# Kernel tuning notes

Measured on AMD Instinct MI355X. Metric: run time of the kernel, lower is better.

## Reference

```python
import jax, jax.numpy as jnp
import numpy as np

N_NODES = 50000


def gcn_conv(x, W, b, row, col, n):
    """PyG GCNConv with default add_self_loops=True, normalize=True.
    out[i] = sum_{e: col[e]=i} d^-1/2[row[e]] d^-1/2[i] * (x@W)[row[e]]
             + d^-1[i]*(x@W)[i] + b,  where d = in-degree + 1 (self-loop).
    """
    x_lin = x @ W                                   # [n, out_ch]
    ones = jnp.ones(row.shape[0], dtype=x.dtype)
    deg = jax.ops.segment_sum(ones, col, num_segments=n) + 1.0  # self-loop
    dinv = jax.lax.rsqrt(deg)                       # deg >= 1, safe
    norm = dinv[row] * dinv[col]                    # [E]
    msg = norm[:, None] * x_lin[row]                # [E, out_ch]
    agg = jax.ops.segment_sum(msg, col, num_segments=n)
    self_term = (dinv * dinv)[:, None] * x_lin      # self-loop contribution
    return agg + self_term + b


def setup_inputs() -> dict:
    key = jax.random.key(0)
    ks = jax.random.split(key, 10)
    in_ch, hid, out_ch = 128, 256, 64
    E = 800000
    x = jax.random.normal(ks[0], (N_NODES, in_ch), dtype=jnp.float32)
    edge_attr = jax.random.normal(ks[1], (E, 8), dtype=jnp.float32)  # unused by forward
    edge_index = jax.random.randint(ks[2], (2, E), 0, N_NODES, dtype=jnp.int64)
    def glorot(k, fan_in, fan_out):
        s = float(np.sqrt(6.0 / (fan_in + fan_out)))
        return jax.random.uniform(k, (fan_in, fan_out), jnp.float32, -s, s)
    return {
        "x": x,
        "edge_attr": edge_attr,
        "edge_index": edge_index,
        "W1": glorot(ks[3], in_ch, hid), "b1": jnp.zeros((hid,), jnp.float32),
        "W2": glorot(ks[4], hid, hid),  "b2": jnp.zeros((hid,), jnp.float32),
        "W3": glorot(ks[5], hid, out_ch), "b3": jnp.zeros((out_ch,), jnp.float32),
    }


def reference(x, edge_attr, edge_index, W1, b1, W2, b2, W3, b3):
    n = x.shape[0]
    row, col = edge_index[0], edge_index[1]
    h = jax.nn.sigmoid(gcn_conv(x, W1, b1, row, col, n))
    h = jax.nn.sigmoid(gcn_conv(h, W2, b2, row, col, n))
    # dropout(p=0.1) in eval mode is identity
    return gcn_conv(h, W3, b3, row, col, n)
```

## Files before the change

### kernel.cpp

```cpp
#include <hip/hip_runtime.h>
#include <hip/hip_bf16.h>

typedef __bf16 bf16x8_t __attribute__((ext_vector_type(8)));
typedef float f32x4_t __attribute__((ext_vector_type(4)));
typedef float f32x2_t __attribute__((ext_vector_type(2)));

__device__ __forceinline__ float bits2f(unsigned int u) {
    union { unsigned int u; float f; } c; c.u = u; return c.f;
}
__device__ __forceinline__ unsigned short f2bf_bits(float f) {
    __hip_bfloat16 h = __float2bfloat16(f);
    return __builtin_bit_cast(unsigned short, h);
}
__device__ __forceinline__ f32x2_t unpack_bf2(unsigned int u) {
    return (f32x2_t){bits2f(u << 16), bits2f(u & 0xffff0000u)};
}
__device__ __forceinline__ int get_xcd() {
    unsigned v;
    asm volatile("s_getreg_b32 %0, hwreg(HW_REG_XCC_ID)" : "=s"(v));
    return (int)(v & 7);
}

__global__ void sentinel_fill(float* __restrict__ out, int n) {
    int i = blockIdx.x * blockDim.x + threadIdx.x;
    if (i < n) out[i] = 100.0f;
}

__global__ void init_combo(const unsigned int* __restrict__ ei, int* __restrict__ flags,
                           unsigned* __restrict__ cnt8, int Mln) {
    if (blockIdx.x == 0) {
        if (threadIdx.x < 64) {
            int lane = threadIdx.x;
            int cz = 0;
            #pragma unroll
            for (int j = 0; j < 4; ++j) {
                int idx = lane * 4 + j;
                cz += (ei[2 * idx + 1] == 0u);
            }
            #pragma unroll
            for (int off = 32; off; off >>= 1) cz += __shfl_down(cz, off);
            if (lane == 0) flags[0] = (cz > 200);
        }
    } else {
        int i = (blockIdx.x - 1) * 256 + threadIdx.x;
        if (i < Mln) cnt8[i] = 0u;
    }
}

__global__ void count_rank_xcd(const int* __restrict__ ei, unsigned* __restrict__ cnt8,
                               int* __restrict__ rank, int* __restrict__ c32,
                               int* __restrict__ r32, unsigned char* __restrict__ xcd8,
                               int E, int M, const int* __restrict__ flags) {
    int e = blockIdx.x * 256 + threadIdx.x;
    int xcd = get_xcd();
    if (e < E) {
        int r, c;
        if (flags[0]) { r = ei[2 * e]; c = ei[2 * E + 2 * e]; }
        else          { r = ei[e];     c = ei[E + e]; }
        c32[e] = c;
        r32[e] = r;
        xcd8[e] = (unsigned char)xcd;
        int rk = 0;
        if ((unsigned)c < (unsigned)M)
            rk = (int)__hip_atomic_fetch_add(&cnt8[(size_t)xcd * M + c], 1u,
                                             __ATOMIC_RELAXED, __HIP_MEMORY_SCOPE_WORKGROUP);
        rank[e] = rk;
    }
}

__global__ void scan_blocks_x(const unsigned* __restrict__ cnt8, unsigned* __restrict__ base8,
                              int* __restrict__ tot, int* __restrict__ excl,
                              int* __restrict__ bsum, int M) {
    int tid = threadIdx.x;
    int i = blockIdx.x * 256 + tid;
    int lane = tid & 63, wv = tid >> 6;
    __shared__ int ws[4];
    int v = 0;
    if (i < M) {
        unsigned run = 0;
        #pragma unroll
        for (int x = 0; x < 8; ++x) {
            unsigned cv = cnt8[(size_t)x * M + i];
            base8[(size_t)x * M + i] = run;
            run += cv;
        }
        v = (int)run;
        tot[i] = v;
    }
    int s = v;
    #pragma unroll
    for (int off = 1; off < 64; off <<= 1) {
        int t = __shfl_up(s, off);
        if (lane >= off) s += t;
    }
    if (lane == 63) ws[wv] = s;
    __syncthreads();
    if (tid == 0) { int a = 0; for (int q = 0; q < 4; ++q) { int t = ws[q]; ws[q] = a; a += t; } }
    __syncthreads();
    int ex = s - v + ws[wv];
    if (i < M) excl[i] = ex;
    if (tid == 255) bsum[blockIdx.x] = ex + v;
}

__global__ void scan_bsums(const int* __restrict__ bsum, int* __restrict__ boff,
                           int nb, int* __restrict__ colptr, int n) {
    int tid = threadIdx.x, lane = tid & 63, wv = tid >> 6;
    __shared__ int ws[4];
    __shared__ int carry;
    if (tid == 0) carry = 0;
    __syncthreads();
    for (int base = 0; base < nb; base += 256) {
        int i = base + tid;
        int v = (i < nb) ? bsum[i] : 0;
        int s = v;
        #pragma unroll
        for (int off = 1; off < 64; off <<= 1) {
            int t = __shfl_up(s, off);
            if (lane >= off) s += t;
        }
        if (lane == 63) ws[wv] = s;
        __syncthreads();
        if (tid == 0) { int a = carry; for (int q = 0; q < 4; ++q) { int t = ws[q]; ws[q] = a; a += t; } carry = a; }
        __syncthreads();
        int ex = s - v + ws[wv];
        if (i < nb) boff[i] = ex;
        __syncthreads();
    }
    if (tid == 0) colptr[n] = carry;
}

__global__ void scan_add_dinv(const int* __restrict__ excl, const int* __restrict__ boff,
                              const int* __restrict__ tot, int* __restrict__ colptr,
                              float* __restrict__ dinv, int n) {
    int i = blockIdx.x * 256 + threadIdx.x;
    if (i < n) {
        colptr[i] = excl[i] + boff[blockIdx.x];
        dinv[i] = rsqrtf((float)tot[i] + 1.0f);
    }
}

__global__ void fill_csr_part2(const int* __restrict__ c32, const int* __restrict__ r32,
                               const unsigned char* __restrict__ xcd8,
                               const unsigned* __restrict__ base8,
                               const int* __restrict__ colptr, const int* __restrict__ rank,
                               int* __restrict__ esrc, int E, int M, int psz) {
    int part = blockIdx.x & 7;
    int e = (blockIdx.x >> 3) * 256 + threadIdx.x;
    int lo = part * psz;
    int hi = lo + psz; if (hi > M) hi = M;
    if (e < E) {
        int c = c32[e];
        if (c >= lo && c < hi) {
            int r = r32[e];
            if ((unsigned)r < (unsigned)M) {
                int p = colptr[c] + (int)base8[(size_t)xcd8[e] * M + c] + rank[e];
                if ((unsigned)p < (unsigned)E) esrc[p] = r;
            }
        }
    }
}

__global__ void prep_fused(const float* __restrict__ x, const float* __restrict__ dinv,
                           unsigned char* __restrict__ xs8,
                           const float* __restrict__ W1, const float* __restrict__ W2,
                           const float* __restrict__ W3,
                           unsigned short* __restrict__ Wt1, unsigned short* __restrict__ Wt2,
                           unsigned short* __restrict__ Wt3,
                           int M, int nps) {
    if ((int)blockIdx.x < nps) {
        int i = blockIdx.x * 256 + threadIdx.x;
        if (i < M * 32) {
            int row = i >> 5;
            float dv = dinv[row];
            float4 v = *(const float4*)(x + (size_t)i * 4);
            unsigned u = __builtin_amdgcn_cvt_pk_fp8_f32(v.x * dv, v.y * dv, 0, false);
            u = __builtin_amdgcn_cvt_pk_fp8_f32(v.z * dv, v.w * dv, u, true);
            *(unsigned*)(xs8 + (size_t)i * 4) = u;
        }
    } else {
        int i = ((int)blockIdx.x - nps) * 256 + threadIdx.x;
        if (i < 32768) {
            int k = i >> 8, n = i & 255;
            Wt1[n * 128 + k] = f2bf_bits(W1[i]);
        } else if (i < 32768 + 65536) {
            int j = i - 32768;
            int k = j >> 8, n = j & 255;
            Wt2[n * 256 + k] = f2bf_bits(W2[j]);
        } else if (i < 114688) {
            int j = i - 98304;
            int k = j >> 6, n = j & 63;
            Wt3[n * 256 + k] = f2bf_bits(W3[j]);
        }
    }
}

template<int K, int BN, int NTOT, int EPI>
__global__ __launch_bounds__(256) void gemm_tile(
    const __bf16* __restrict__ A,
    const unsigned short* __restrict__ Bt,
    const float* __restrict__ dinv,
    const float* __restrict__ bias,
    void* __restrict__ Y,
    int M)
{
    constexpr int KS = (K > 128) ? 128 : K;
    constexpr int KP = KS + 8;
    constexpr int NT = BN / 2 / 16;
    __shared__ unsigned short Bs[BN * KP];

    const int tid  = threadIdx.x;
    const int lane = tid & 63;
    const int wave = tid >> 6;
    const int wm   = wave >> 1;
    const int wn   = wave & 1;
    const int quad = lane >> 4;
    const int l16  = lane & 15;
    const int n0   = blockIdx.y * BN;

    int mrow[4];
#pragma unroll
    for (int mt = 0; mt < 4; ++mt) {
        int r = blockIdx.x * 128 + wm * 64 + mt * 16 + l16;
        mrow[mt] = (r < M) ? r : (M - 1);
    }

    f32x4_t acc[4][NT];
#pragma unroll
    for (int mt = 0; mt < 4; ++mt)
#pragma unroll
        for (int t = 0; t < NT; ++t) acc[mt][t] = (f32x4_t){0.f, 0.f, 0.f, 0.f};

    const unsigned short* BsW = &Bs[(wn * (BN / 2)) * KP];

    for (int kh = 0; kh < K; kh += KS) {
        constexpr int CH = BN * KS / 8;
        for (int idx = tid; idx < CH; idx += 256) {
            int n  = idx / (KS / 8);
            int k8 = idx - n * (KS / 8);
            uint4 v = *(const uint4*)(Bt + (size_t)(n0 + n) * K + kh + k8 * 8);
            *(uint4*)&Bs[n * KP + k8 * 8] = v;
        }
        __syncthreads();

#pragma unroll
        for (int kc = 0; kc < KS; kc += 32) {
            bf16x8_t a[4], b[NT];
#pragma unroll
            for (int mt = 0; mt < 4; ++mt)
                a[mt] = *(const bf16x8_t*)(A + (size_t)mrow[mt] * K + kh + kc + quad * 8);
#pragma unroll
            for (int t = 0; t < NT; ++t)
                b[t] = *(const bf16x8_t*)&BsW[(t * 16 + l16) * KP + kc + quad * 8];
#pragma unroll
            for (int mt = 0; mt < 4; ++mt)
#pragma unroll
                for (int t = 0; t < NT; ++t)
                    acc[mt][t] = __builtin_amdgcn_mfma_f32_16x16x32_bf16(a[mt], b[t], acc[mt][t], 0, 0, 0);
        }
        if (kh + KS < K) __syncthreads();
    }

    float bv[NT];
    if constexpr (EPI == 1) {
#pragma unroll
        for (int t = 0; t < NT; ++t)
            bv[t] = bias[n0 + wn * (BN / 2) + t * 16 + l16];
    }

#pragma unroll
    for (int mt = 0; mt < 4; ++mt) {
        int rowbase = blockIdx.x * 128 + wm * 64 + mt * 16 + quad * 4;
#pragma unroll
        for (int r = 0; r < 4; ++r) {
            int rrow = rowbase + r;
            if (rrow < M) {
                if constexpr (EPI == 0) {
                    float dv = dinv[rrow];
#pragma unroll
                    for (int t = 0; t < NT; ++t) {
                        int ccol = n0 + wn * (BN / 2) + t * 16 + l16;
                        ((__hip_bfloat16*)Y)[(size_t)rrow * NTOT + ccol] =
                            __float2bfloat16(acc[mt][t][r] * dv);
                    }
                } else if constexpr (EPI == 1) {
#pragma unroll
                    for (int t = 0; t < NT; ++t) {
                        int ccol = n0 + wn * (BN / 2) + t * 16 + l16;
                        float o = acc[mt][t][r] + bv[t];
                        o = 1.f / (1.f + __expf(-o));
                        ((__hip_bfloat16*)Y)[(size_t)rrow * NTOT + ccol] = __float2bfloat16(o);
                    }
                } else {
                    float dv = dinv[rrow];
#pragma unroll
                    for (int t = 0; t < NT; ++t) {
                        int ccol = n0 + wn * (BN / 2) + t * 16 + l16;
                        float o = acc[mt][t][r] * dv;
                        int pk = __builtin_amdgcn_cvt_pk_fp8_f32(o, o, 0, false);
                        ((unsigned char*)Y)[(size_t)rrow * NTOT + ccol] = (unsigned char)(pk & 0xff);
                    }
                }
            }
        }
    }
}

__global__ __launch_bounds__(256) void aggregate_fp8_v4(
    const unsigned char* __restrict__ Y8,
    const int* __restrict__ colptr,
    const int* __restrict__ esrc,
    const float* __restrict__ dinv,
    const float* __restrict__ bias,
    unsigned short* __restrict__ H,
    int M, int Etot)
{
    const int lane = threadIdx.x & 63;
    const int wave = threadIdx.x >> 6;
    int node = blockIdx.x * 4 + wave;
    if (node >= M) return;

    int s = colptr[node];
    int e = colptr[node + 1];
    if (s < 0) s = 0;
    if (e > Etot) e = Etot;
    if (e < s) e = s;
    int n = e - s;

    const char* Yb = (const char*)Y8;
    const unsigned lb = (unsigned)(lane * 4);

    unsigned su = *(const unsigned*)(Yb + (((unsigned)node) << 8) + lb);

    f32x2_t a0 = {0.f, 0.f}, a1 = {0.f, 0.f};

    auto gather8 = [&](unsigned* u, int base) {
        #pragma unroll
        for (int k = 0; k < 8; ++k) {
            unsigned off = (((unsigned)esrc[s + base + k]) << 8) + lb;
            u[k] = *(const unsigned*)(Yb + off);
        }
    };
    auto acc8 = [&](const unsigned* u) {
        #pragma unroll
        for (int k = 0; k < 8; ++k) {
            a0 += __builtin_amdgcn_cvt_pk_f32_fp8(u[k], false);
            a1 += __builtin_amdgcn_cvt_pk_f32_fp8(u[k], true);
        }
    };

    unsigned ua[8], ub[8];
    int NB = n >> 3;
    if (NB > 0) {
        gather8(ua, 0);
        int i = 1;
        for (; i + 1 < NB; i += 2) {
            gather8(ub, i << 3);
            acc8(ua);
            gather8(ua, (i + 1) << 3);
            acc8(ub);
        }
        if (i < NB) {
            gather8(ub, i << 3);
            acc8(ua);
            acc8(ub);
        } else {
            acc8(ua);
        }
    }
    #pragma unroll 2
    for (int t = NB << 3; t < n; ++t) {
        unsigned off = (((unsigned)esrc[s + t]) << 8) + lb;
        unsigned u = *(const unsigned*)(Yb + off);
        a0 += __builtin_amdgcn_cvt_pk_f32_fp8(u, false);
        a1 += __builtin_amdgcn_cvt_pk_f32_fp8(u, true);
    }
    a0 += __builtin_amdgcn_cvt_pk_f32_fp8(su, false);
    a1 += __builtin_amdgcn_cvt_pk_f32_fp8(su, true);

    float dv = dinv[node];
    float4 bv = *(const float4*)(bias + lane * 4);
    float o0 = a0[0] * dv + bv.x;
    float o1 = a0[1] * dv + bv.y;
    float o2 = a1[0] * dv + bv.z;
    float o3 = a1[1] * dv + bv.w;
    o0 = 1.f / (1.f + __expf(-o0));
    o1 = 1.f / (1.f + __expf(-o1));
    o2 = 1.f / (1.f + __expf(-o2));
    o3 = 1.f / (1.f + __expf(-o3));
    uint2 st;
    st.x = (unsigned)f2bf_bits(o0) | ((unsigned)f2bf_bits(o1) << 16);
    st.y = (unsigned)f2bf_bits(o2) | ((unsigned)f2bf_bits(o3) << 16);
    *(uint2*)(H + (size_t)node * 256 + lane * 4) = st;
}

__global__ __launch_bounds__(256) void aggregate_xs8b(
    const unsigned char* __restrict__ X8,
    const int* __restrict__ colptr,
    const int* __restrict__ esrc,
    const float* __restrict__ dinv,
    unsigned short* __restrict__ xa,
    int M, int Etot)
{
    const int lane = threadIdx.x & 63;
    const int wave = threadIdx.x >> 6;
    const int l4 = lane & 15;
    const int g4 = lane >> 4;
    int node = blockIdx.x * 4 + wave;
    if (node >= M) return;

    int s = colptr[node];
    int e = colptr[node + 1];
    if (s < 0) s = 0;
    if (e > Etot) e = Etot;
    if (e < s) e = s;
    int n = e - s;

    const char* Yb = (const char*)X8;
    const unsigned lb = (unsigned)(l4 * 8);

    uint2 su = {0u, 0u};
    if (g4 == 0) su = *(const uint2*)(Yb + ((unsigned)node) * 128u + lb);

    f32x2_t a0 = {0.f, 0.f}, a1 = {0.f, 0.f}, a2 = {0.f, 0.f}, a3 = {0.f, 0.f};

    auto gat = [&](uint2* u, int base) {
        u[0] = *(const uint2*)(Yb + ((unsigned)esrc[s + base + g4]) * 128u + lb);
        u[1] = *(const uint2*)(Yb + ((unsigned)esrc[s + base + 4 + g4]) * 128u + lb);
    };
    auto acc = [&](const uint2* u) {
        #pragma unroll
        for (int k = 0; k < 2; ++k) {
            a0 += __builtin_amdgcn_cvt_pk_f32_fp8(u[k].x, false);
            a1 += __builtin_amdgcn_cvt_pk_f32_fp8(u[k].x, true);
            a2 += __builtin_amdgcn_cvt_pk_f32_fp8(u[k].y, false);
            a3 += __builtin_amdgcn_cvt_pk_f32_fp8(u[k].y, true);
        }
    };

    uint2 ua[2], ub[2];
    int NB = n >> 3;
    if (NB > 0) {
        gat(ua, 0);
        int i = 1;
        for (; i + 1 < NB; i += 2) {
            gat(ub, i << 3); acc(ua);
            gat(ua, (i + 1) << 3); acc(ub);
        }
        if (i < NB) { gat(ub, i << 3); acc(ua); acc(ub); }
        else acc(ua);
    }
    for (int t = NB << 3; t < n; t += 4) {
        if (t + g4 < n) {
            uint2 u = *(const uint2*)(Yb + ((unsigned)esrc[s + t + g4]) * 128u + lb);
            a0 += __builtin_amdgcn_cvt_pk_f32_fp8(u.x, false);
            a1 += __builtin_amdgcn_cvt_pk_f32_fp8(u.x, true);
            a2 += __builtin_amdgcn_cvt_pk_f32_fp8(u.y, false);
            a3 += __builtin_amdgcn_cvt_pk_f32_fp8(u.y, true);
        }
    }
    if (g4 == 0) {
        a0 += __builtin_amdgcn_cvt_pk_f32_fp8(su.x, false);
        a1 += __builtin_amdgcn_cvt_pk_f32_fp8(su.x, true);
        a2 += __builtin_amdgcn_cvt_pk_f32_fp8(su.y, false);
        a3 += __builtin_amdgcn_cvt_pk_f32_fp8(su.y, true);
    }

    #pragma unroll
    for (int off = 16; off < 64; off <<= 1) {
        a0[0] += __shfl_xor(a0[0], off); a0[1] += __shfl_xor(a0[1], off);
        a1[0] += __shfl_xor(a1[0], off); a1[1] += __shfl_xor(a1[1], off);
        a2[0] += __shfl_xor(a2[0], off); a2[1] += __shfl_xor(a2[1], off);
        a3[0] += __shfl_xor(a3[0], off); a3[1] += __shfl_xor(a3[1], off);
    }

    if (g4 == 0) {
        float dv = dinv[node];
        uint4 st;
        st.x = (unsigned)f2bf_bits(a0[0] * dv) | ((unsigned)f2bf_bits(a0[1] * dv) << 16);
        st.y = (unsigned)f2bf_bits(a1[0] * dv) | ((unsigned)f2bf_bits(a1[1] * dv) << 16);
        st.z = (unsigned)f2bf_bits(a2[0] * dv) | ((unsigned)f2bf_bits(a2[1] * dv) << 16);
        st.w = (unsigned)f2bf_bits(a3[0] * dv) | ((unsigned)f2bf_bits(a3[1] * dv) << 16);
        *(uint4*)(xa + (size_t)node * 128 + l4 * 8) = st;
    }
}

__global__ __launch_bounds__(256) void aggregate_bf16_64_v5(
    const unsigned short* __restrict__ Yin,
    const int* __restrict__ colptr,
    const int* __restrict__ esrc,
    const float* __restrict__ dinv,
    const float* __restrict__ bias,
    float* __restrict__ out,
    int M, int Etot)
{
    const int lane = threadIdx.x & 63;
    const int wave = threadIdx.x >> 6;
    const int l4 = lane & 15;
    const int g4 = lane >> 4;
    int node = blockIdx.x * 4 + wave;
    if (node >= M) return;

    int s = colptr[node];
    int e = colptr[node + 1];
    if (s < 0) s = 0;
    if (e > Etot) e = Etot;
    if (e < s) e = s;
    int n = e - s;

    const char* Yb = (const char*)Yin;
    const unsigned lb = (unsigned)(l4 * 8);

    uint2 su = {0u, 0u};
    if (g4 == 0) su = *(const uint2*)(Yb + ((unsigned)node) * 128u + lb);

    f32x2_t a0 = {0.f, 0.f}, a1 = {0.f, 0.f};

    auto gat = [&](uint2* u, int base) {
        u[0] = *(const uint2*)(Yb + ((unsigned)esrc[s + base + g4]) * 128u + lb);
        u[1] = *(const uint2*)(Yb + ((unsigned)esrc[s + base + 4 + g4]) * 128u + lb);
    };
    auto acc = [&](const uint2* u) {
        #pragma unroll
        for (int k = 0; k < 2; ++k) {
            a0 += unpack_bf2(u[k].x);
            a1 += unpack_bf2(u[k].y);
        }
    };

    uint2 ua[2], ub[2];
    int NB = n >> 3;
    if (NB > 0) {
        gat(ua, 0);
        int i = 1;
        for (; i + 1 < NB; i += 2) {
            gat(ub, i << 3); acc(ua);
            gat(ua, (i + 1) << 3); acc(ub);
        }
        if (i < NB) { gat(ub, i << 3); acc(ua); acc(ub); }
        else acc(ua);
    }
    for (int t = NB << 3; t < n; t += 4) {
        if (t + g4 < n) {
            uint2 u = *(const uint2*)(Yb + ((unsigned)esrc[s + t + g4]) * 128u + lb);
            a0 += unpack_bf2(u.x);
            a1 += unpack_bf2(u.y);
        }
    }
    if (g4 == 0) {
        a0 += unpack_bf2(su.x);
        a1 += unpack_bf2(su.y);
    }

    #pragma unroll
    for (int off = 16; off < 64; off <<= 1) {
        a0[0] += __shfl_xor(a0[0], off); a0[1] += __shfl_xor(a0[1], off);
        a1[0] += __shfl_xor(a1[0], off); a1[1] += __shfl_xor(a1[1], off);
    }

    if (g4 == 0) {
        float dv = dinv[node];
        float4 bv = *(const float4*)(bias + l4 * 4);
        float4 st;
        st.x = a0[0] * dv + bv.x;
        st.y = a0[1] * dv + bv.y;
        st.z = a1[0] * dv + bv.z;
        st.w = a1[1] * dv + bv.w;
        *(float4*)(out + (size_t)node * 64 + l4 * 4) = st;
    }
}


extern "C" void kernel_launch(void* const* d_in, const int* in_sizes, int n_in,
                              void* d_out, int out_size, void* d_ws, size_t ws_size,
                              hipStream_t stream)
{
    int iEI = 2, iW1 = 3, iB1 = 4, iW2 = 5, iB2 = 6, iW3 = 7, iB3 = 8;
    if (n_in == 8) { iEI = 1; iW1 = 2; iB1 = 3; iW2 = 4; iB2 = 5; iW3 = 6; iB3 = 7; }

    const float* x  = (const float*)d_in[0];
    const int* ei   = (const int*)d_in[iEI];
    const float* W1 = (const float*)d_in[iW1];
    const float* b1 = (const float*)d_in[iB1];
    const float* W2 = (const float*)d_in[iW2];
    const float* b2 = (const float*)d_in[iB2];
    const float* W3 = (const float*)d_in[iW3];
    const float* b3 = (const float*)d_in[iB3];

    const int M = in_sizes[0] / 128;
    const int E = in_sizes[iEI] / 2;
    const int NB = (M + 255) / 256;
    const int PSZ = (M + 7) / 8;

    auto rnd = [](size_t b) { return (b + 255) & ~(size_t)255; };
    size_t needed = rnd(64 * 4)
                  + rnd((size_t)M * 4)
                  + rnd((size_t)M * 32) * 2
                  + rnd((size_t)M * 4)
                  + rnd((size_t)(M + 1) * 4)
                  + rnd((size_t)M * 4)
                  + rnd((size_t)(NB + 1) * 4) * 2
                  + rnd((size_t)E * 4) * 4
                  + rnd((size_t)E)
                  + rnd((size_t)256 * 128 * 2)
                  + rnd((size_t)256 * 256 * 2)
                  + rnd((size_t)64 * 256 * 2)
                  + rnd((size_t)M * 256 * 2) * 2;
    if (ws_size < needed) {
        sentinel_fill<<<(out_size + 255) / 256, 256, 0, stream>>>((float*)d_out, out_size);
        return;
    }

    char* p = (char*)d_ws;
    auto alloc = [&](size_t bytes) {
        char* r = p;
        p += (bytes + 255) & ~(size_t)255;
        return r;
    };
    int* flags  = (int*)alloc(64 * 4);
    float* dinv = (float*)alloc((size_t)M * 4);
    unsigned* cnt8  = (unsigned*)alloc((size_t)M * 32);
    unsigned* base8 = (unsigned*)alloc((size_t)M * 32);
    int* tot    = (int*)alloc((size_t)M * 4);
    int* colptr = (int*)alloc((size_t)(M + 1) * 4);
    int* excl   = (int*)alloc((size_t)M * 4);
    int* bsum   = (int*)alloc((size_t)(NB + 1) * 4);
    int* boff   = (int*)alloc((size_t)(NB + 1) * 4);
    int* esrc   = (int*)alloc((size_t)E * 4);
    int* rank   = (int*)alloc((size_t)E * 4);
    int* c32    = (int*)alloc((size_t)E * 4);
    int* r32    = (int*)alloc((size_t)E * 4);
    unsigned char* xcd8 = (unsigned char*)alloc((size_t)E);
    unsigned short* Wt1 = (unsigned short*)alloc((size_t)256 * 128 * 2);
    unsigned short* Wt2 = (unsigned short*)alloc((size_t)256 * 256 * 2);
    unsigned short* Wt3 = (unsigned short*)alloc((size_t)64 * 256 * 2);
    __hip_bfloat16* ybuf = (__hip_bfloat16*)alloc((size_t)M * 256 * 2);
    __hip_bfloat16* hbuf = (__hip_bfloat16*)alloc((size_t)M * 256 * 2);

    unsigned char* xs8 = (unsigned char*)ybuf;
    unsigned short* xa = (unsigned short*)ybuf + (size_t)M * 128;
    unsigned char*  y8 = (unsigned char*)ybuf;

    int Mln = M * 8;
    init_combo<<<(Mln + 255) / 256 + 1, 256, 0, stream>>>(
        (const unsigned int*)ei, flags, cnt8, Mln);

    count_rank_xcd<<<(E + 255) / 256, 256, 0, stream>>>(
        ei, cnt8, rank, c32, r32, xcd8, E, M, flags);
    scan_blocks_x<<<NB, 256, 0, stream>>>(cnt8, base8, tot, excl, bsum, M);
    scan_bsums<<<1, 256, 0, stream>>>(bsum, boff, NB, colptr, M);
    scan_add_dinv<<<NB, 256, 0, stream>>>(excl, boff, tot, colptr, dinv, M);
    fill_csr_part2<<<((E + 255) / 256) * 8, 256, 0, stream>>>(
        c32, r32, xcd8, base8, colptr, rank, esrc, E, M, PSZ);

    int gmb = (M + 127) / 128;
    int ga  = (M + 3) / 4;
    int nps = (M * 32 + 255) / 256;

    prep_fused<<<nps + 448, 256, 0, stream>>>(
        x, dinv, xs8, W1, W2, W3, Wt1, Wt2, Wt3, M, nps);

    aggregate_xs8b<<<ga, 256, 0, stream>>>(
        xs8, colptr, esrc, dinv, xa, M, E);
    gemm_tile<128, 128, 256, 1><<<dim3(gmb, 2), 256, 0, stream>>>(
        (const __bf16*)xa, Wt1, dinv, b1, hbuf, M);
    gemm_tile<256, 128, 256, 2><<<dim3(gmb, 2), 256, 0, stream>>>(
        (const __bf16*)hbuf, Wt2, dinv, b2, y8, M);
    aggregate_fp8_v4<<<ga, 256, 0, stream>>>(
        y8, colptr, esrc, dinv, b2, (unsigned short*)hbuf, M, E);
    gemm_tile<256, 64, 64, 0><<<dim3(gmb, 1), 256, 0, stream>>>(
        (const __bf16*)hbuf, Wt3, dinv, b3, ybuf, M);
    aggregate_bf16_64_v5<<<ga, 256, 0, stream>>>(
        (const unsigned short*)ybuf, colptr, esrc, dinv, b3, (float*)d_out, M, E);
}
```

Measured before the change: 327.1 us.

## Fuse CSR fill into prep kernel and drop XCD-partitioned edge scatter

Merges the CSR edge-source fill into the x/weight preparation kernel, so one launch covers both jobs through disjoint block ranges. The fill previously launched 8x the blocks and had each partition handle only destination columns in its range, keeping scattered writes local to one XCD's cache. Now each edge is handled by exactly one block, which cuts redundant index loads and one launch. The cost is losing that per-XCD write locality for the esrc scatter.

```diff
diff --git a/kernel.cpp b/kernel.cpp
--- a/kernel.cpp
+++ b/kernel.cpp
@@ -139,36 +139,34 @@
     }
 }
 
-__global__ void fill_csr_part2(const int* __restrict__ c32, const int* __restrict__ r32,
-                               const unsigned char* __restrict__ xcd8,
-                               const unsigned* __restrict__ base8,
-                               const int* __restrict__ colptr, const int* __restrict__ rank,
-                               int* __restrict__ esrc, int E, int M, int psz) {
-    int part = blockIdx.x & 7;
-    int e = (blockIdx.x >> 3) * 256 + threadIdx.x;
-    int lo = part * psz;
-    int hi = lo + psz; if (hi > M) hi = M;
-    if (e < E) {
-        int c = c32[e];
-        if (c >= lo && c < hi) {
-            int r = r32[e];
-            if ((unsigned)r < (unsigned)M) {
-                int p = colptr[c] + (int)base8[(size_t)xcd8[e] * M + c] + rank[e];
-                if ((unsigned)p < (unsigned)E) esrc[p] = r;
+__global__ void fill_prep_fused(
+    const int* __restrict__ c32, const int* __restrict__ r32,
+    const unsigned char* __restrict__ xcd8, const unsigned* __restrict__ base8,
+    const int* __restrict__ colptr, const int* __restrict__ rank,
+    int* __restrict__ esrc, int E,
+    const float* __restrict__ x, const float* __restrict__ dinv,
+    unsigned char* __restrict__ xs8,
+    const float* __restrict__ W1, const float* __restrict__ W2,
+    const float* __restrict__ W3,
+    unsigned short* __restrict__ Wt1, unsigned short* __restrict__ Wt2,
+    unsigned short* __restrict__ Wt3,
+    int M, int nfe, int nps)
+{
+    int b = (int)blockIdx.x;
+    if (b < nfe) {
+        int e = b * 256 + threadIdx.x;
+        if (e < E) {
+            int c = c32[e];
+            if ((unsigned)c < (unsigned)M) {
+                int r = r32[e];
+                if ((unsigned)r < (unsigned)M) {
+                    int p = colptr[c] + (int)base8[(size_t)xcd8[e] * M + c] + rank[e];
+                    if ((unsigned)p < (unsigned)E) esrc[p] = r;
+                }
             }
         }
-    }
-}
-
-__global__ void prep_fused(const float* __restrict__ x, const float* __restrict__ dinv,
-                           unsigned char* __restrict__ xs8,
-                           const float* __restrict__ W1, const float* __restrict__ W2,
-                           const float* __restrict__ W3,
-                           unsigned short* __restrict__ Wt1, unsigned short* __restrict__ Wt2,
-                           unsigned short* __restrict__ Wt3,
-                           int M, int nps) {
-    if ((int)blockIdx.x < nps) {
-        int i = blockIdx.x * 256 + threadIdx.x;
+    } else if (b < nfe + nps) {
+        int i = (b - nfe) * 256 + threadIdx.x;
         if (i < M * 32) {
             int row = i >> 5;
             float dv = dinv[row];
@@ -178,7 +176,7 @@
             *(unsigned*)(xs8 + (size_t)i * 4) = u;
         }
     } else {
-        int i = ((int)blockIdx.x - nps) * 256 + threadIdx.x;
+        int i = (b - nfe - nps) * 256 + threadIdx.x;
         if (i < 32768) {
             int k = i >> 8, n = i & 255;
             Wt1[n * 128 + k] = f2bf_bits(W1[i]);
@@ -589,7 +587,6 @@
     const int M = in_sizes[0] / 128;
     const int E = in_sizes[iEI] / 2;
     const int NB = (M + 255) / 256;
-    const int PSZ = (M + 7) / 8;
 
     auto rnd = [](size_t b) { return (b + 255) & ~(size_t)255; };
     size_t needed = rnd(64 * 4)
@@ -649,15 +646,15 @@
     scan_blocks_x<<<NB, 256, 0, stream>>>(cnt8, base8, tot, excl, bsum, M);
     scan_bsums<<<1, 256, 0, stream>>>(bsum, boff, NB, colptr, M);
     scan_add_dinv<<<NB, 256, 0, stream>>>(excl, boff, tot, colptr, dinv, M);
-    fill_csr_part2<<<((E + 255) / 256) * 8, 256, 0, stream>>>(
-        c32, r32, xcd8, base8, colptr, rank, esrc, E, M, PSZ);
 
     int gmb = (M + 127) / 128;
     int ga  = (M + 3) / 4;
+    int nfe = (E + 255) / 256;
     int nps = (M * 32 + 255) / 256;
 
-    prep_fused<<<nps + 448, 256, 0, stream>>>(
-        x, dinv, xs8, W1, W2, W3, Wt1, Wt2, Wt3, M, nps);
+    fill_prep_fused<<<nfe + nps + 448, 256, 0, stream>>>(
+        c32, r32, xcd8, base8, colptr, rank, esrc, E,
+        x, dinv, xs8, W1, W2, W3, Wt1, Wt2, Wt3, M, nfe, nps);
 
     aggregate_xs8b<<<ga, 256, 0, stream>>>(
         xs8, colptr, esrc, dinv, xa, M, E);
```

After: 315.7 us. 3.5% less time.
